# Kernel tuning notes

Measured on AMD Instinct MI355X. Metric: run time of the kernel, lower is better.

Reference implementation:

```python
import jax, jax.numpy as jnp
import numpy as np

N, E = 50000, 600000
DIN, DMID, DATTR, DOUT, DEMB, DH, K = 128, 128, 32, 128, 256, 768, 16


def setup_inputs() -> dict:
    key = jax.random.key(0)
    ks = jax.random.split(key, 12)
    s = lambda d: 1.0 / np.sqrt(d)
    return {
        "x": jax.random.normal(ks[0], (N, DIN), jnp.float32),
        "attributes": jax.random.normal(ks[1], (N, DATTR), jnp.float32),
        "edge_weight": jax.random.uniform(ks[2], (E,), jnp.float32),
        "hidden_state": jax.random.normal(ks[3], (1, DH), jnp.float32),
        "edge_index": jax.random.randint(ks[4], (2, E), 0, N, jnp.int64),
        "W1": jax.random.normal(ks[5], (DIN, DMID), jnp.float32) * s(DIN),
        "b1": jnp.zeros((DMID,), jnp.float32),
        "W2": jax.random.normal(ks[6], (DMID + DATTR, DOUT), jnp.float32) * s(DMID + DATTR),
        "b2": jnp.zeros((DOUT,), jnp.float32),
        "Wmap": jax.random.normal(ks[7], (DOUT + DATTR, DEMB), jnp.float32) * s(DOUT + DATTR),
        "bmap": jnp.zeros((DEMB,), jnp.float32),
        "Wattn": jax.random.normal(ks[8], (DH, DOUT + DATTR), jnp.float32) * s(DH),
    }


def gcn_conv(x, W, b, src, dst, w, n):
    """PyG GCNConv with normalize=True: A_hat = D^-1/2 (A+I) D^-1/2, out = A_hat X W + b."""
    loop = jnp.arange(n, dtype=src.dtype)
    src2 = jnp.concatenate([src, loop])
    dst2 = jnp.concatenate([dst, loop])
    w2 = jnp.concatenate([w, jnp.ones((n,), x.dtype)])
    deg = jax.ops.segment_sum(w2, dst2, num_segments=n)
    dinv = jnp.where(deg > 0, jax.lax.rsqrt(jnp.maximum(deg, 1e-12)), 0.0)
    norm = dinv[src2] * w2 * dinv[dst2]        # [E+N]
    h = x @ W                                   # [n, out] transform first (small dim)
    msg = h[src2] * norm[:, None]               # gather + scale, [E+N, out]
    return jax.ops.segment_sum(msg, dst2, num_segments=n) + b


def reference(x, attributes, edge_weight, hidden_state, edge_index,
              W1, b1, W2, b2, Wmap, bmap, Wattn):
    n = x.shape[0]
    src, dst = edge_index[0], edge_index[1]
    h = jax.nn.relu(gcn_conv(x, W1, b1, src, dst, edge_weight, n))
    # F.dropout with training=False is identity (module run in eval mode)
    h = jnp.concatenate([h, attributes], axis=1)           # [N, DMID+DATTR]
    h = gcn_conv(h, W2, b2, src, dst, edge_weight, n)      # [N, DOUT]
    h = jnp.concatenate([h, attributes], axis=1)           # [N, DOUT+DATTR]
    # DotAttnChoseImportentNode: project hidden state, dot with node feats, take top-K nodes
    q = hidden_state @ Wattn                                # [1, DOUT+DATTR]
    scores = h @ q[0]                                       # [N]
    _, idx = jax.lax.top_k(scores, K)
    chose_nodes = h[idx].reshape(1, -1)                     # [1, K*(DOUT+DATTR)]
    # final_mapping: mean-pool graph embed + linear
    emb = jnp.mean(h, axis=0, keepdims=True) @ Wmap + bmap  # [1, DEMB]
    return jnp.concatenate([emb, chose_nodes], axis=1)      # [1, DEMB + K*(DOUT+DATTR)]
```

## Files before the change

kernel.cpp:

```cpp
#include <hip/hip_runtime.h>

#define N_NODES 50000
#define N_EDGES 600000
#define D_IN 128
#define D_MID 128
#define D_ATTR 32
#define D_OUT 128
#define D_EMB 256
#define D_H 768
#define K_TOP 16
#define D_CAT (D_OUT + D_ATTR)
#define N_CHUNKBLKS 196
#define N_CAND (N_CHUNKBLKS * K_TOP)
#define CSLOTS 13
#define WSCALE 262144.0f
#define CS_BLOCKS 768

__global__ void k_init(unsigned long long* packed, float* q) {
    int i = blockIdx.x * blockDim.x + threadIdx.x;
    if (i < N_NODES) packed[i] = 0ULL;
    if (i < D_CAT)   q[i] = 0.0f;
}

__global__ void k_deg(const int* __restrict__ dst, const float* __restrict__ w,
                      unsigned long long* __restrict__ packed) {
    int e = blockIdx.x * blockDim.x + threadIdx.x;
    if (e < N_EDGES) {
        int d = dst[e];
        unsigned long long q = (1ULL << 40)
                             + (unsigned long long)__float2uint_rn(w[e] * WSCALE);
        atomicAdd(&packed[d], q);
    }
}

__global__ __launch_bounds__(256) void k_scan_blk(const unsigned long long* __restrict__ packed,
                                                  float* __restrict__ dinv,
                                                  int* __restrict__ incl,
                                                  int* __restrict__ bsum) {
    __shared__ int sm[256];
    int tid = threadIdx.x;
    int i = blockIdx.x * 256 + tid;
    unsigned long long p = (i < N_NODES) ? packed[i] : 0ULL;
    int v = (int)(p >> 40);
    if (i < N_NODES) {
        float wsum = (float)(p & 0xFFFFFFFFFFULL) * (1.0f / WSCALE);
        dinv[i] = rsqrtf(1.0f + wsum);
    }
    sm[tid] = v;
    __syncthreads();
    for (int off = 1; off < 256; off <<= 1) {
        int t = (tid >= off) ? sm[tid - off] : 0;
        __syncthreads();
        sm[tid] += t;
        __syncthreads();
    }
    if (i < N_NODES) incl[i] = sm[tid];
    if (tid == 255) bsum[blockIdx.x] = sm[255];
}

__global__ __launch_bounds__(256) void k_scan_top(const int* __restrict__ bsum,
                                                  int* __restrict__ boff) {
    __shared__ int sm[256];
    int tid = threadIdx.x;
    int v = (tid < N_CHUNKBLKS) ? bsum[tid] : 0;
    sm[tid] = v;
    __syncthreads();
    for (int off = 1; off < 256; off <<= 1) {
        int t = (tid >= off) ? sm[tid - off] : 0;
        __syncthreads();
        sm[tid] += t;
        __syncthreads();
    }
    if (tid < N_CHUNKBLKS) boff[tid] = sm[tid] - v;
}

__global__ __launch_bounds__(256) void k_scan_add(const int* __restrict__ incl,
                                                  const int* __restrict__ boff,
                                                  const unsigned long long* __restrict__ packed,
                                                  int* __restrict__ row_ptr,
                                                  int* __restrict__ cursor) {
    int i = blockIdx.x * 256 + threadIdx.x;
    if (i < N_NODES) {
        int ip = incl[i] + boff[blockIdx.x];
        row_ptr[i + 1] = ip;
        cursor[i] = ip - (int)(packed[i] >> 40);
        if (i == 0) row_ptr[0] = 0;
    }
}

__global__ void k_fill(const int* __restrict__ src, const int* __restrict__ dst,
                       const float* __restrict__ w, const float* __restrict__ dinv,
                       int* __restrict__ cursor, int2* __restrict__ recs) {
    int e = blockIdx.x * blockDim.x + threadIdx.x;
    if (e < N_EDGES) {
        int s = src[e], d = dst[e];
        int pos = atomicAdd(&cursor[d], 1);
        float nr = dinv[s] * w[e] * dinv[d];
        recs[pos] = make_int2(s, __float_as_int(nr));
    }
}

#define GBM 64
#define GBK 32
__global__ __launch_bounds__(256) void k_gemm(
    const float* __restrict__ in1, int d1,
    const float* __restrict__ in2, int d2,
    const float* __restrict__ W,
    float* __restrict__ out)
{
    __shared__ float xs[GBM][GBK + 1];
    __shared__ float ws[GBK][128];
    int tid = threadIdx.x;
    int cx = tid & 7;
    int ry = tid >> 3;
    int row0 = blockIdx.x * GBM;
    float acc[2][16];
#pragma unroll
    for (int i = 0; i < 2; ++i)
#pragma unroll
        for (int j = 0; j < 16; ++j) acc[i][j] = 0.0f;
    int KD = d1 + d2;
    for (int kt = 0; kt < KD; kt += GBK) {
        const float* srcp; int sd, scol;
        if (kt < d1) { srcp = in1; sd = d1; scol = kt; }
        else         { srcp = in2; sd = d2; scol = kt - d1; }
#pragma unroll
        for (int i = 0; i < 2; ++i) {
            int vid = tid + i * 256;
            int rr = vid >> 3;
            int kc = (vid & 7) * 4;
            int r = row0 + rr;
            float4 val = make_float4(0.f, 0.f, 0.f, 0.f);
            if (r < N_NODES)
                val = *(const float4*)(srcp + (size_t)r * sd + scol + kc);
            xs[rr][kc + 0] = val.x;
            xs[rr][kc + 1] = val.y;
            xs[rr][kc + 2] = val.z;
            xs[rr][kc + 3] = val.w;
        }
#pragma unroll
        for (int i = 0; i < 4; ++i) {
            int vid = tid + i * 256;
            int kk = vid >> 5;
            int c = (vid & 31) * 4;
            *(float4*)&ws[kk][c] = *(const float4*)(W + (size_t)(kt + kk) * 128 + c);
        }
        __syncthreads();
#pragma unroll
        for (int kk = 0; kk < GBK; ++kk) {
            float xv0 = xs[ry * 2 + 0][kk];
            float xv1 = xs[ry * 2 + 1][kk];
            float wv[16];
#pragma unroll
            for (int j4 = 0; j4 < 4; ++j4)
                *(float4*)&wv[j4 * 4] = *(float4*)&ws[kk][cx * 4 + j4 * 32];
#pragma unroll
            for (int j = 0; j < 16; ++j) {
                acc[0][j] += xv0 * wv[j];
                acc[1][j] += xv1 * wv[j];
            }
        }
        __syncthreads();
    }
#pragma unroll
    for (int i = 0; i < 2; ++i) {
        int r = row0 + ry * 2 + i;
        if (r < N_NODES) {
#pragma unroll
            for (int j4 = 0; j4 < 4; ++j4)
                *(float4*)(out + (size_t)r * 128 + cx * 4 + j4 * 32)
                    = *(float4*)&acc[i][j4 * 4];
        }
    }
}

__global__ __launch_bounds__(256) void k_agg(
    const float* __restrict__ t, const float* __restrict__ dinv,
    const int* __restrict__ row_ptr, const int2* __restrict__ recs,
    const float* __restrict__ bias,
    float* __restrict__ out, int relu_flag,
    const float* __restrict__ attr, const float* __restrict__ q,
    float* __restrict__ scores, int score_flag)
{
    int lane = threadIdx.x & 63;
    int node = blockIdx.x * 4 + (threadIdx.x >> 6);
    if (node >= N_NODES) return;
    const float2* t2 = (const float2*)t;
    float di = dinv[node];
    float sw = di * di;
    float2 v = t2[(size_t)node * 64 + lane];
    float accx = v.x * sw, accy = v.y * sw;
    int e0 = row_ptr[node], e1 = row_ptr[node + 1];
    int len = e1 - e0;
    for (int base = 0; base < len; base += 64) {
        int m = len - base; if (m > 64) m = 64;
        int2 myrec = make_int2(0, 0);
        if (lane < m) myrec = recs[e0 + base + lane];
        int j = 0;
        for (; j + 8 <= m; j += 8) {
            int   s0 = __shfl(myrec.x, j + 0, 64), s1 = __shfl(myrec.x, j + 1, 64);
            int   s2 = __shfl(myrec.x, j + 2, 64), s3 = __shfl(myrec.x, j + 3, 64);
            int   s4 = __shfl(myrec.x, j + 4, 64), s5 = __shfl(myrec.x, j + 5, 64);
            int   s6 = __shfl(myrec.x, j + 6, 64), s7 = __shfl(myrec.x, j + 7, 64);
            float w0 = __int_as_float(__shfl(myrec.y, j + 0, 64));
            float w1 = __int_as_float(__shfl(myrec.y, j + 1, 64));
            float w2 = __int_as_float(__shfl(myrec.y, j + 2, 64));
            float w3 = __int_as_float(__shfl(myrec.y, j + 3, 64));
            float w4 = __int_as_float(__shfl(myrec.y, j + 4, 64));
            float w5 = __int_as_float(__shfl(myrec.y, j + 5, 64));
            float w6 = __int_as_float(__shfl(myrec.y, j + 6, 64));
            float w7 = __int_as_float(__shfl(myrec.y, j + 7, 64));
            float2 u0 = t2[(size_t)s0 * 64 + lane];
            float2 u1 = t2[(size_t)s1 * 64 + lane];
            float2 u2 = t2[(size_t)s2 * 64 + lane];
            float2 u3 = t2[(size_t)s3 * 64 + lane];
            float2 u4 = t2[(size_t)s4 * 64 + lane];
            float2 u5 = t2[(size_t)s5 * 64 + lane];
            float2 u6 = t2[(size_t)s6 * 64 + lane];
            float2 u7 = t2[(size_t)s7 * 64 + lane];
            accx += w0 * u0.x + w1 * u1.x + w2 * u2.x + w3 * u3.x
                  + w4 * u4.x + w5 * u5.x + w6 * u6.x + w7 * u7.x;
            accy += w0 * u0.y + w1 * u1.y + w2 * u2.y + w3 * u3.y
                  + w4 * u4.y + w5 * u5.y + w6 * u6.y + w7 * u7.y;
        }
        for (; j + 4 <= m; j += 4) {
            int s0 = __shfl(myrec.x, j + 0, 64);
            int s1 = __shfl(myrec.x, j + 1, 64);
            int s2 = __shfl(myrec.x, j + 2, 64);
            int s3 = __shfl(myrec.x, j + 3, 64);
            float w0 = __int_as_float(__shfl(myrec.y, j + 0, 64));
            float w1 = __int_as_float(__shfl(myrec.y, j + 1, 64));
            float w2 = __int_as_float(__shfl(myrec.y, j + 2, 64));
            float w3 = __int_as_float(__shfl(myrec.y, j + 3, 64));
            float2 u0 = t2[(size_t)s0 * 64 + lane];
            float2 u1 = t2[(size_t)s1 * 64 + lane];
            float2 u2 = t2[(size_t)s2 * 64 + lane];
            float2 u3 = t2[(size_t)s3 * 64 + lane];
            accx += w0 * u0.x + w1 * u1.x + w2 * u2.x + w3 * u3.x;
            accy += w0 * u0.y + w1 * u1.y + w2 * u2.y + w3 * u3.y;
        }
        for (; j < m; ++j) {
            int s = __shfl(myrec.x, j, 64);
            float wn = __int_as_float(__shfl(myrec.y, j, 64));
            float2 u = t2[(size_t)s * 64 + lane];
            accx += wn * u.x;
            accy += wn * u.y;
        }
    }
    const float2* b2 = (const float2*)bias;
    float2 bb = b2[lane];
    accx += bb.x; accy += bb.y;
    if (relu_flag) {
        accx = fmaxf(accx, 0.0f);
        accy = fmaxf(accy, 0.0f);
    }
    float2 res; res.x = accx; res.y = accy;
    ((float2*)out)[(size_t)node * 64 + lane] = res;
    if (score_flag) {
        const float2* q2 = (const float2*)q;
        float2 qq = q2[lane];
        float s = accx * qq.x + accy * qq.y;
        if (lane < 16) {
            const float2* at2 = (const float2*)attr;
            float2 a = at2[(size_t)node * 16 + lane];
            float2 qa = q2[64 + lane];
            s += a.x * qa.x + a.y * qa.y;
        }
        for (int off = 32; off; off >>= 1) s += __shfl_xor(s, off, 64);
        if (lane == 0) scores[node] = s;
    }
}

__global__ void k_q(const float* __restrict__ hs, const float* __restrict__ Wattn,
                    float* __restrict__ q) {
    int j = threadIdx.x;
    if (j >= D_CAT) return;
    int k0 = blockIdx.x * (D_H / 8);
    float acc = 0.0f;
    for (int k = k0; k < k0 + D_H / 8; k++) acc += hs[k] * Wattn[k * D_CAT + j];
    atomicAdd(&q[j], acc);
}

__global__ __launch_bounds__(256) void k_colsum_partial(const float* __restrict__ h2,
                                                        const float* __restrict__ attr,
                                                        float* __restrict__ partial) {
    __shared__ float4 sm[256];
    int tid = threadIdx.x;
    int per = (N_NODES + CS_BLOCKS - 1) / CS_BLOCKS;
    int r0 = blockIdx.x * per;
    int r1 = min(N_NODES, r0 + per);
    float* myrow = partial + (size_t)blockIdx.x * D_CAT;
    {
        const float4* h4 = (const float4*)h2;
        int c = tid & 31;
        float4 acc = make_float4(0.f, 0.f, 0.f, 0.f);
        for (int r = r0 + (tid >> 5); r < r1; r += 8) {
            float4 v = h4[(size_t)r * 32 + c];
            acc.x += v.x; acc.y += v.y; acc.z += v.z; acc.w += v.w;
        }
        sm[tid] = acc;
        __syncthreads();
        if (tid < 32) {
            float4 s = sm[tid];
#pragma unroll
            for (int g = 1; g < 8; ++g) {
                float4 v = sm[g * 32 + tid];
                s.x += v.x; s.y += v.y; s.z += v.z; s.w += v.w;
            }
            ((float4*)myrow)[tid] = s;
        }
        __syncthreads();
    }
    {
        const float4* a4 = (const float4*)attr;
        int c = tid & 7;
        float4 acc = make_float4(0.f, 0.f, 0.f, 0.f);
        for (int r = r0 + (tid >> 3); r < r1; r += 32) {
            float4 v = a4[(size_t)r * 8 + c];
            acc.x += v.x; acc.y += v.y; acc.z += v.z; acc.w += v.w;
        }
        sm[tid] = acc;
        __syncthreads();
        if (tid < 8) {
            float4 s = sm[tid];
#pragma unroll
            for (int g = 1; g < 32; ++g) {
                float4 v = sm[g * 8 + tid];
                s.x += v.x; s.y += v.y; s.z += v.z; s.w += v.w;
            }
            ((float4*)(myrow + D_OUT))[tid] = s;
        }
    }
}

__global__ __launch_bounds__(256) void k_colsum_reduce(const float* __restrict__ partial,
                                                       float* __restrict__ colsum) {
    __shared__ float4 sm[256];
    int tid = threadIdx.x;
    int cg = blockIdx.x;
    float4 acc = make_float4(0.f, 0.f, 0.f, 0.f);
#pragma unroll
    for (int k = 0; k < 3; ++k) {
        int b = tid + k * 256;
        float4 v = *(const float4*)(partial + (size_t)b * D_CAT + cg * 4);
        acc.x += v.x; acc.y += v.y; acc.z += v.z; acc.w += v.w;
    }
    sm[tid] = acc;
    __syncthreads();
    for (int off = 128; off; off >>= 1) {
        if (tid < off) {
            float4 v = sm[tid + off];
            sm[tid].x += v.x; sm[tid].y += v.y; sm[tid].z += v.z; sm[tid].w += v.w;
        }
        __syncthreads();
    }
    if (tid == 0) *(float4*)(colsum + cg * 4) = sm[0];
}

__global__ __launch_bounds__(256) void k_top1(const float* __restrict__ scores,
                                              float* __restrict__ cand_s,
                                              int* __restrict__ cand_i) {
    int tid = threadIdx.x;
    int lane = tid & 63;
    int wave = tid >> 6;
    int i = blockIdx.x * 256 + tid;
    float s = (i < N_NODES) ? scores[i] : -INFINITY;
    int ix = i;
    __shared__ float wls[4];
    __shared__ int   wli[4];
    __shared__ int   fin_i;
    for (int it = 0; it < K_TOP; ++it) {
        float bs = s; int bi = ix;
#pragma unroll
        for (int off = 32; off; off >>= 1) {
            float s2 = __shfl_xor(bs, off, 64);
            int   i2 = __shfl_xor(bi, off, 64);
            if (s2 > bs || (s2 == bs && i2 < bi)) { bs = s2; bi = i2; }
        }
        if (lane == 0) { wls[wave] = bs; wli[wave] = bi; }
        __syncthreads();
        if (tid == 0) {
            float f = wls[0]; int fi = wli[0];
#pragma unroll
            for (int w = 1; w < 4; ++w)
                if (wls[w] > f || (wls[w] == f && wli[w] < fi)) { f = wls[w]; fi = wli[w]; }
            cand_s[blockIdx.x * K_TOP + it] = f;
            cand_i[blockIdx.x * K_TOP + it] = fi;
            fin_i = fi;
        }
        __syncthreads();
        if (ix == fin_i) s = -INFINITY;
    }
}

__global__ __launch_bounds__(256) void k_top2emb(
    const float* __restrict__ cand_s, const int* __restrict__ cand_i,
    const float* __restrict__ colsum, const float* __restrict__ Wmap,
    const float* __restrict__ bmap,
    const float* __restrict__ h2, const float* __restrict__ attr,
    float* __restrict__ out)
{
    float s[CSLOTS]; int ix[CSLOTS];
    int tid = threadIdx.x;
    int lane = tid & 63;
    int wave = tid >> 6;
#pragma unroll
    for (int j = 0; j < CSLOTS; ++j) {
        int c = tid + j * 256;
        s[j]  = (c < N_CAND) ? cand_s[c] : -INFINITY;
        ix[j] = (c < N_CAND) ? cand_i[c] : 0x7fffffff;
    }
    __shared__ float wsum_s[4];
    __shared__ int   wsum_i[4];
    __shared__ int   win_i;
    __shared__ int   ti[K_TOP];
    for (int it = 0; it < K_TOP; ++it) {
        float bs = -INFINITY; int bi = 0x7fffffff;
#pragma unroll
        for (int j = 0; j < CSLOTS; ++j) {
            if (s[j] > bs || (s[j] == bs && ix[j] < bi)) { bs = s[j]; bi = ix[j]; }
        }
#pragma unroll
        for (int off = 32; off; off >>= 1) {
            float s2 = __shfl_xor(bs, off, 64);
            int   i2 = __shfl_xor(bi, off, 64);
            if (s2 > bs || (s2 == bs && i2 < bi)) { bs = s2; bi = i2; }
        }
        if (lane == 0) { wsum_s[wave] = bs; wsum_i[wave] = bi; }
        __syncthreads();
        if (tid == 0) {
            float ws0 = wsum_s[0]; int wi0 = wsum_i[0];
#pragma unroll
            for (int w = 1; w < 4; ++w) {
                float s2 = wsum_s[w]; int i2 = wsum_i[w];
                if (s2 > ws0 || (s2 == ws0 && i2 < wi0)) { ws0 = s2; wi0 = i2; }
            }
            win_i = wi0;
            ti[it] = wi0;
        }
        __syncthreads();
        int w = win_i;
#pragma unroll
        for (int j = 0; j < CSLOTS; ++j)
            if (ix[j] == w) s[j] = -INFINITY;
        __syncthreads();
    }
    __shared__ float cs[D_CAT];
    if (tid < D_CAT) cs[tid] = colsum[tid];
    __syncthreads();
    float acc = 0.0f;
#pragma unroll 8
    for (int k = 0; k < D_CAT; ++k) acc += cs[k] * Wmap[k * D_EMB + tid];
    out[tid] = acc * (1.0f / N_NODES) + bmap[tid];
    for (int idx = tid; idx < K_TOP * D_CAT; idx += 256) {
        int kk = idx / D_CAT;
        int d = idx % D_CAT;
        int node = ti[kk];
        out[D_EMB + idx] = (d < D_OUT) ? h2[node * D_OUT + d]
                                       : attr[node * D_ATTR + (d - D_OUT)];
    }
}

extern "C" void kernel_launch(void* const* d_in, const int* in_sizes, int n_in,
                              void* d_out, int out_size, void* d_ws, size_t ws_size,
                              hipStream_t stream) {
    const float* x      = (const float*)d_in[0];
    const float* attr   = (const float*)d_in[1];
    const float* ew     = (const float*)d_in[2];
    const float* hs     = (const float*)d_in[3];
    const int*   ei     = (const int*)d_in[4];
    const float* W1     = (const float*)d_in[5];
    const float* b1     = (const float*)d_in[6];
    const float* W2     = (const float*)d_in[7];
    const float* b2     = (const float*)d_in[8];
    const float* Wmap   = (const float*)d_in[9];
    const float* bmap   = (const float*)d_in[10];
    const float* Wattn  = (const float*)d_in[11];
    float* out = (float*)d_out;
    const int* e_src = ei;
    const int* e_dst = ei + N_EDGES;

    size_t off = 0;
    auto alloc = [&](size_t bytes) {
        void* p = (char*)d_ws + off;
        off += (bytes + 255) / 256 * 256;
        return p;
    };
    unsigned long long* packed = (unsigned long long*)alloc((size_t)N_NODES * 8);
    float* dinv   = (float*)alloc((size_t)N_NODES * 4);
    int*   rowp   = (int*)  alloc((size_t)(N_NODES + 1) * 4);
    int*   cursor = (int*)  alloc((size_t)N_NODES * 4);
    int2*  recs   = (int2*) alloc((size_t)N_EDGES * 8);
    float* bufA   = (float*)alloc((size_t)N_NODES * 128 * 4);
    float* bufB   = (float*)alloc((size_t)N_NODES * 128 * 4);
    float* scores = (float*)alloc((size_t)N_NODES * 4);
    float* q      = (float*)alloc(D_CAT * 4);
    float* colsum = (float*)alloc(D_CAT * 4);
    float* partial= (float*)alloc((size_t)CS_BLOCKS * D_CAT * 4);
    float* cand_s = (float*)alloc((size_t)N_CAND * 4);
    int*   cand_i = (int*)  alloc((size_t)N_CAND * 4);
    int*   incl   = (int*)  alloc((size_t)N_NODES * 4);
    int*   bsum   = (int*)  alloc((size_t)N_CHUNKBLKS * 4);
    int*   boff   = (int*)  alloc((size_t)N_CHUNKBLKS * 4);

    int nblk = (N_NODES + 255) / 256;
    int eblk = (N_EDGES + 255) / 256;

    hipLaunchKernelGGL(k_init, dim3(nblk), dim3(256), 0, stream, packed, q);
    hipLaunchKernelGGL(k_deg, dim3(eblk), dim3(256), 0, stream, e_dst, ew, packed);
    hipLaunchKernelGGL(k_scan_blk, dim3(nblk), dim3(256), 0, stream, packed, dinv, incl, bsum);
    hipLaunchKernelGGL(k_scan_top, dim3(1), dim3(256), 0, stream, bsum, boff);
    hipLaunchKernelGGL(k_scan_add, dim3(nblk), dim3(256), 0, stream, incl, boff, packed,
                       rowp, cursor);
    hipLaunchKernelGGL(k_fill, dim3(eblk), dim3(256), 0, stream, e_src, e_dst, ew, dinv,
                       cursor, recs);
    hipLaunchKernelGGL(k_q, dim3(8), dim3(192), 0, stream, hs, Wattn, q);
    hipLaunchKernelGGL(k_gemm, dim3((N_NODES + GBM - 1) / GBM), dim3(256), 0, stream,
                       x, D_IN, x, 0, W1, bufA);
    hipLaunchKernelGGL(k_agg, dim3((N_NODES + 3) / 4), dim3(256), 0, stream,
                       bufA, dinv, rowp, recs, b1, bufB, 1,
                       (const float*)nullptr, (const float*)nullptr, (float*)nullptr, 0);
    hipLaunchKernelGGL(k_gemm, dim3((N_NODES + GBM - 1) / GBM), dim3(256), 0, stream,
                       bufB, D_MID, attr, D_ATTR, W2, bufA);
    hipLaunchKernelGGL(k_agg, dim3((N_NODES + 3) / 4), dim3(256), 0, stream,
                       bufA, dinv, rowp, recs, b2, bufB, 0,
                       attr, q, scores, 1);
    hipLaunchKernelGGL(k_colsum_partial, dim3(CS_BLOCKS), dim3(256), 0, stream,
                       bufB, attr, partial);
    hipLaunchKernelGGL(k_colsum_reduce, dim3(D_CAT / 4), dim3(256), 0, stream,
                       partial, colsum);
    hipLaunchKernelGGL(k_top1, dim3(N_CHUNKBLKS), dim3(256), 0, stream,
                       scores, cand_s, cand_i);
    hipLaunchKernelGGL(k_top2emb, dim3(1), dim3(256), 0, stream,
                       cand_s, cand_i, colsum, Wmap, bmap, bufB, attr, out);
}
```

Baseline: 302.5 us.

## Derive CSR slots from degree-atomic ranks and move scoring into colsum pass

The degree-counting atomic now returns the old count, which is stored as each edge's rank within its destination row. The fill kernel then computes its slot as row_ptr plus rank, with no second atomic pass over a cursor array. Attention score computation moves out of the second aggregation kernel into the column-sum kernel, which already reads every row of h and the attributes. This removes one contended atomic per edge and the score work in aggregation, at the cost of an extra 2.4MB rank array and a dependence on the colsum kernel's row ordering for scores.

```diff
diff --git a/kernel.cpp b/kernel.cpp
--- a/kernel.cpp
+++ b/kernel.cpp
@@ -23,13 +23,14 @@
 }
 
 __global__ void k_deg(const int* __restrict__ dst, const float* __restrict__ w,
-                      unsigned long long* __restrict__ packed) {
+                      unsigned long long* __restrict__ packed, int* __restrict__ rank) {
     int e = blockIdx.x * blockDim.x + threadIdx.x;
     if (e < N_EDGES) {
         int d = dst[e];
-        unsigned long long q = (1ULL << 40)
-                             + (unsigned long long)__float2uint_rn(w[e] * WSCALE);
-        atomicAdd(&packed[d], q);
+        unsigned long long qv = (1ULL << 40)
+                              + (unsigned long long)__float2uint_rn(w[e] * WSCALE);
+        unsigned long long old = atomicAdd(&packed[d], qv);
+        rank[e] = (int)(old >> 40);
     }
 }
 
@@ -76,25 +77,22 @@
 
 __global__ __launch_bounds__(256) void k_scan_add(const int* __restrict__ incl,
                                                   const int* __restrict__ boff,
-                                                  const unsigned long long* __restrict__ packed,
-                                                  int* __restrict__ row_ptr,
-                                                  int* __restrict__ cursor) {
+                                                  int* __restrict__ row_ptr) {
     int i = blockIdx.x * 256 + threadIdx.x;
     if (i < N_NODES) {
-        int ip = incl[i] + boff[blockIdx.x];
-        row_ptr[i + 1] = ip;
-        cursor[i] = ip - (int)(packed[i] >> 40);
+        row_ptr[i + 1] = incl[i] + boff[blockIdx.x];
         if (i == 0) row_ptr[0] = 0;
     }
 }
 
 __global__ void k_fill(const int* __restrict__ src, const int* __restrict__ dst,
-                       const float* __restrict__ w, const float* __restrict__ dinv,
-                       int* __restrict__ cursor, int2* __restrict__ recs) {
+                       const float* __restrict__ w, const int* __restrict__ rank,
+                       const float* __restrict__ dinv, const int* __restrict__ rowp,
+                       int2* __restrict__ recs) {
     int e = blockIdx.x * blockDim.x + threadIdx.x;
     if (e < N_EDGES) {
         int s = src[e], d = dst[e];
-        int pos = atomicAdd(&cursor[d], 1);
+        int pos = rowp[d] + rank[e];
         float nr = dinv[s] * w[e] * dinv[d];
         recs[pos] = make_int2(s, __float_as_int(nr));
     }
@@ -178,9 +176,7 @@
     const float* __restrict__ t, const float* __restrict__ dinv,
     const int* __restrict__ row_ptr, const int2* __restrict__ recs,
     const float* __restrict__ bias,
-    float* __restrict__ out, int relu_flag,
-    const float* __restrict__ attr, const float* __restrict__ q,
-    float* __restrict__ scores, int score_flag)
+    float* __restrict__ out, int relu_flag)
 {
     int lane = threadIdx.x & 63;
     int node = blockIdx.x * 4 + (threadIdx.x >> 6);
@@ -256,19 +252,6 @@
     }
     float2 res; res.x = accx; res.y = accy;
     ((float2*)out)[(size_t)node * 64 + lane] = res;
-    if (score_flag) {
-        const float2* q2 = (const float2*)q;
-        float2 qq = q2[lane];
-        float s = accx * qq.x + accy * qq.y;
-        if (lane < 16) {
-            const float2* at2 = (const float2*)attr;
-            float2 a = at2[(size_t)node * 16 + lane];
-            float2 qa = q2[64 + lane];
-            s += a.x * qa.x + a.y * qa.y;
-        }
-        for (int off = 32; off; off >>= 1) s += __shfl_xor(s, off, 64);
-        if (lane == 0) scores[node] = s;
-    }
 }
 
 __global__ void k_q(const float* __restrict__ hs, const float* __restrict__ Wattn,
@@ -281,10 +264,13 @@
     atomicAdd(&q[j], acc);
 }
 
-__global__ __launch_bounds__(256) void k_colsum_partial(const float* __restrict__ h2,
-                                                        const float* __restrict__ attr,
-                                                        float* __restrict__ partial) {
+__global__ __launch_bounds__(256) void k_post(const float* __restrict__ h2,
+                                              const float* __restrict__ attr,
+                                              const float* __restrict__ q,
+                                              float* __restrict__ partial,
+                                              float* __restrict__ scores) {
     __shared__ float4 sm[256];
+    __shared__ float rowsc[80];
     int tid = threadIdx.x;
     int per = (N_NODES + CS_BLOCKS - 1) / CS_BLOCKS;
     int r0 = blockIdx.x * per;
@@ -293,10 +279,15 @@
     {
         const float4* h4 = (const float4*)h2;
         int c = tid & 31;
+        float4 qv = ((const float4*)q)[c];
         float4 acc = make_float4(0.f, 0.f, 0.f, 0.f);
         for (int r = r0 + (tid >> 5); r < r1; r += 8) {
             float4 v = h4[(size_t)r * 32 + c];
             acc.x += v.x; acc.y += v.y; acc.z += v.z; acc.w += v.w;
+            float sd = v.x * qv.x + v.y * qv.y + v.z * qv.z + v.w * qv.w;
+#pragma unroll
+            for (int off = 16; off; off >>= 1) sd += __shfl_xor(sd, off, 32);
+            if (c == 0) rowsc[r - r0] = sd;
         }
         sm[tid] = acc;
         __syncthreads();
@@ -314,10 +305,15 @@
     {
         const float4* a4 = (const float4*)attr;
         int c = tid & 7;
+        float4 qv = ((const float4*)q)[32 + c];
         float4 acc = make_float4(0.f, 0.f, 0.f, 0.f);
         for (int r = r0 + (tid >> 3); r < r1; r += 32) {
             float4 v = a4[(size_t)r * 8 + c];
             acc.x += v.x; acc.y += v.y; acc.z += v.z; acc.w += v.w;
+            float sd = v.x * qv.x + v.y * qv.y + v.z * qv.z + v.w * qv.w;
+#pragma unroll
+            for (int off = 4; off; off >>= 1) sd += __shfl_xor(sd, off, 8);
+            if (c == 0) scores[r] = rowsc[r - r0] + sd;
         }
         sm[tid] = acc;
         __syncthreads();
@@ -489,7 +485,7 @@
     unsigned long long* packed = (unsigned long long*)alloc((size_t)N_NODES * 8);
     float* dinv   = (float*)alloc((size_t)N_NODES * 4);
     int*   rowp   = (int*)  alloc((size_t)(N_NODES + 1) * 4);
-    int*   cursor = (int*)  alloc((size_t)N_NODES * 4);
+    int*   rank   = (int*)  alloc((size_t)N_EDGES * 4);
     int2*  recs   = (int2*) alloc((size_t)N_EDGES * 8);
     float* bufA   = (float*)alloc((size_t)N_NODES * 128 * 4);
     float* bufB   = (float*)alloc((size_t)N_NODES * 128 * 4);
@@ -507,26 +503,23 @@
     int eblk = (N_EDGES + 255) / 256;
 
     hipLaunchKernelGGL(k_init, dim3(nblk), dim3(256), 0, stream, packed, q);
-    hipLaunchKernelGGL(k_deg, dim3(eblk), dim3(256), 0, stream, e_dst, ew, packed);
+    hipLaunchKernelGGL(k_deg, dim3(eblk), dim3(256), 0, stream, e_dst, ew, packed, rank);
     hipLaunchKernelGGL(k_scan_blk, dim3(nblk), dim3(256), 0, stream, packed, dinv, incl, bsum);
     hipLaunchKernelGGL(k_scan_top, dim3(1), dim3(256), 0, stream, bsum, boff);
-    hipLaunchKernelGGL(k_scan_add, dim3(nblk), dim3(256), 0, stream, incl, boff, packed,
-                       rowp, cursor);
-    hipLaunchKernelGGL(k_fill, dim3(eblk), dim3(256), 0, stream, e_src, e_dst, ew, dinv,
-                       cursor, recs);
+    hipLaunchKernelGGL(k_scan_add, dim3(nblk), dim3(256), 0, stream, incl, boff, rowp);
+    hipLaunchKernelGGL(k_fill, dim3(eblk), dim3(256), 0, stream, e_src, e_dst, ew, rank,
+                       dinv, rowp, recs);
     hipLaunchKernelGGL(k_q, dim3(8), dim3(192), 0, stream, hs, Wattn, q);
     hipLaunchKernelGGL(k_gemm, dim3((N_NODES + GBM - 1) / GBM), dim3(256), 0, stream,
                        x, D_IN, x, 0, W1, bufA);
     hipLaunchKernelGGL(k_agg, dim3((N_NODES + 3) / 4), dim3(256), 0, stream,
-                       bufA, dinv, rowp, recs, b1, bufB, 1,
-                       (const float*)nullptr, (const float*)nullptr, (float*)nullptr, 0);
+                       bufA, dinv, rowp, recs, b1, bufB, 1);
     hipLaunchKernelGGL(k_gemm, dim3((N_NODES + GBM - 1) / GBM), dim3(256), 0, stream,
                        bufB, D_MID, attr, D_ATTR, W2, bufA);
     hipLaunchKernelGGL(k_agg, dim3((N_NODES + 3) / 4), dim3(256), 0, stream,
-                       bufA, dinv, rowp, recs, b2, bufB, 0,
-                       attr, q, scores, 1);
-    hipLaunchKernelGGL(k_colsum_partial, dim3(CS_BLOCKS), dim3(256), 0, stream,
-                       bufB, attr, partial);
+                       bufA, dinv, rowp, recs, b2, bufB, 0);
+    hipLaunchKernelGGL(k_post, dim3(CS_BLOCKS), dim3(256), 0, stream,
+                       bufB, attr, q, partial, scores);
     hipLaunchKernelGGL(k_colsum_reduce, dim3(D_CAT / 4), dim3(256), 0, stream,
                        partial, colsum);
     hipLaunchKernelGGL(k_top1, dim3(N_CHUNKBLKS), dim3(256), 0, stream,
```

Result: faster. 284.4 us (-6.0%).
